# Kernel tuning notes

Hardware: AMD Instinct MI355X
Metric: run time of the kernel (lower is better)

## Reference

```python
import jax, jax.numpy as jnp
import numpy as np

B, C, T = 32, 64, 4096
K = 256  # truncated memory length (kwargs['k'])


def setup_inputs() -> dict:
    key = jax.random.key(0)
    k1, k2 = jax.random.split(key)
    x = jax.random.normal(k1, (B, C, T), dtype=jnp.float32)
    epsilon = jax.random.normal(k2, (), dtype=jnp.float32)
    loc = jnp.asarray(0.5, dtype=jnp.float32)    # alpha_loc parameter
    scale = jnp.asarray(0.1, dtype=jnp.float32)  # alpha_scale parameter (pre-softplus)
    return {"x": x, "loc": loc, "scale": scale, "epsilon": epsilon, "k": K}


def _gl_coeffs(alpha, k, dtype):
    # Grunwald-Letnikov weights: w_0 = 1, w_j = w_{j-1} * (j - 1 - alpha) / j
    j = jnp.arange(k, dtype=dtype)
    factors = jnp.where(j == 0, jnp.asarray(1.0, dtype),
                        (j - 1.0 - alpha) / jnp.maximum(j, 1.0))
    return jnp.cumprod(factors)  # [k]


def reference(x, loc, scale, epsilon, k):
    # reparameterized fractional order (Normal prior): alpha = loc + softplus(scale) * eps
    alpha = loc + jax.nn.softplus(scale) * epsilon
    w = _gl_coeffs(alpha, k, x.dtype)  # [k]
    b, c, t = x.shape
    # truncated GL fractional derivative = causal depthwise conv with k taps:
    # out[n] = sum_{j=0}^{k-1} w_j * x[n-j]
    lhs = x.reshape(b * c, 1, t)                 # [N, 1, T]
    rhs = w[::-1].reshape(1, 1, k)               # [O=1, I=1, K] (flip for correlation)
    out = jax.lax.conv_general_dilated(lhs, rhs, window_strides=(1,),
                                       padding=[(k - 1, 0)])
    return out.reshape(b, c, t)
```

## Files before the change

### kernel.cpp

```cpp
#include <hip/hip_runtime.h>
#include <hip/hip_bf16.h>
#include <hip/hip_fp16.h>

#define TLEN 4096
#define KTAPS 256
#define NT 18
#define WCH 24

typedef __attribute__((ext_vector_type(8))) _Float16 f16x8;
typedef __attribute__((ext_vector_type(4))) unsigned int uint4v;
typedef __attribute__((ext_vector_type(16))) float f32x16;

__global__ void __launch_bounds__(256, 5)
frac_conv_fused2(const float* __restrict__ x,
                 const float* __restrict__ loc,
                 const float* __restrict__ scale,
                 const float* __restrict__ eps,
                 float* __restrict__ out) {
    __shared__ __align__(16) float s[KTAPS];
    __shared__ unsigned int wrevp[320];
    __shared__ __align__(16) unsigned short Bf[WCH * 64 * 8];

    const int tid  = threadIdx.x;
    const int wave = tid >> 6;
    const int lane = tid & 63;
    const int l5   = lane >> 5;
    const int ln   = lane & 31;

    int wgid = blockIdx.x;
    if ((gridDim.x & 7) == 0) {
        const int cpx = gridDim.x >> 3;
        wgid = (blockIdx.x & 7) * cpx + (blockIdx.x >> 3);
    }
    const int rt  = wgid >> 5;
    const int sg  = wgid & 31;
    const int bn0 = sg * 128;

    const int r  = tid >> 3;
    const int cg = tid & 7;
    const float* __restrict__ xrow = x + (size_t)(rt * 32 + r) * TLEN;
    float4 v[12];
    #pragma unroll
    for (int jj = 0; jj < 12; ++jj) {
        const int w0 = cg * 4 + jj * 32;
        const int tg = bn0 - 256 + w0;
        v[jj] = (tg >= 0) ? *(const float4*)(xrow + tg) : make_float4(0.f, 0.f, 0.f, 0.f);
    }

    {
        const float alpha = loc[0] + log1pf(expf(scale[0])) * eps[0];
        const int j0 = 4 * lane;
        const float f0 = (j0 == 0) ? 1.0f : (((float)j0 - 1.0f - alpha) / (float)j0);
        const float f1 = (((float)j0 + 0.0f - alpha) / (float)(j0 + 1));
        const float f2 = (((float)j0 + 1.0f - alpha) / (float)(j0 + 2));
        const float f3 = (((float)j0 + 2.0f - alpha) / (float)(j0 + 3));
        const float p0 = f0, p1 = p0 * f1, p2 = p1 * f2, p3 = p2 * f3;
        float g = p3;
        #pragma unroll
        for (int dlt = 1; dlt < 64; dlt <<= 1) {
            const float t = __shfl_up(g, dlt, 64);
            if (lane >= dlt) g *= t;
        }
        float Sprev = __shfl_up(g, 1, 64);
        if (lane == 0) Sprev = 1.0f;
        if (wave == 0) {
            ((float4*)s)[lane] = make_float4(Sprev * p0, Sprev * p1, Sprev * p2, g);
        }
    }
    __syncthreads();

    {
        const int j = tid;
        const float a = (j >= 32) ? s[287 - j] : 0.0f;
        const float b = (j >= 31) ? s[286 - j] : 0.0f;
        wrevp[j] = __builtin_bit_cast(unsigned int, __builtin_amdgcn_cvt_pkrtz(a, b));
        if (tid < 64) {
            const int j2 = 256 + tid;
            const float a2 = (j2 <= 287) ? s[287 - j2] : 0.0f;
            const float b2 = (j2 <= 286) ? s[286 - j2] : 0.0f;
            wrevp[j2] = __builtin_bit_cast(unsigned int, __builtin_amdgcn_cvt_pkrtz(a2, b2));
        }
    }

    {
        uint2* Bf2 = (uint2*)Bf;
        #pragma unroll
        for (int jj = 0; jj < 12; ++jj) {
            const int w0 = cg * 4 + jj * 32;
            const auto a = __builtin_amdgcn_cvt_pkrtz(v[jj].x, v[jj].y);
            const auto b = __builtin_amdgcn_cvt_pkrtz(v[jj].z, v[jj].w);
            const int c  = w0 >> 4;
            const int h8 = (w0 >> 3) & 1;
            const int e0 = w0 & 7;
            const int uoff = (c * 64 + r + 32 * h8) * 8 + e0;
            Bf2[uoff >> 2] = make_uint2(__builtin_bit_cast(unsigned int, a),
                                        __builtin_bit_cast(unsigned int, b));
        }
    }
    __syncthreads();

    const int n0  = bn0 + wave * 32;
    const int lcb = wave * 2;
    const f16x8* Bv = (const f16x8*)Bf;
    const int o0 = 31 - ln + 8 * l5;

    auto LOADA = [&](int d) -> f16x8 {
        const int o = o0 + 16 * d;
        uint4v u;
        u[0] = wrevp[o];
        u[1] = wrevp[o + 2];
        u[2] = wrevp[o + 4];
        u[3] = wrevp[o + 6];
        return __builtin_bit_cast(f16x8, u);
    };

    f16x8 Afr[NT];
    f16x8 Bfr[NT];
    Bfr[0] = Bv[(lcb + 0) * 64 + lane];
    Bfr[1] = Bv[(lcb + 1) * 64 + lane];
    Bfr[2] = Bv[(lcb + 2) * 64 + lane];
    Bfr[3] = Bv[(lcb + 3) * 64 + lane];
    Afr[0] = LOADA(0);
    Afr[1] = LOADA(1);

    f32x16 acc = {0.f, 0.f, 0.f, 0.f, 0.f, 0.f, 0.f, 0.f,
                  0.f, 0.f, 0.f, 0.f, 0.f, 0.f, 0.f, 0.f};

    #pragma unroll
    for (int d = 0; d < NT; ++d) {
        if (d + 4 < NT) Bfr[d + 4] = Bv[(lcb + d + 4) * 64 + lane];
        if (d + 2 < NT) Afr[d + 2] = LOADA(d + 2);
        acc = __builtin_amdgcn_mfma_f32_32x32x16_f16(Afr[d], Bfr[d], acc, 0, 0, 0);
    }

    float* __restrict__ orow = out + (size_t)(rt * 32 + ln) * TLEN;
    #pragma unroll
    for (int g = 0; g < 4; ++g) {
        *(float4*)(orow + n0 + 8 * g + 4 * l5) =
            make_float4(acc[4 * g + 0], acc[4 * g + 1], acc[4 * g + 2], acc[4 * g + 3]);
    }
}

__global__ void gl_coeff_kernel(const float* __restrict__ loc,
                                const float* __restrict__ scale,
                                const float* __restrict__ eps,
                                float* __restrict__ w_out) {
    __shared__ float s[KTAPS];
    const int j = threadIdx.x;
    const float alpha = loc[0] + log1pf(expf(scale[0])) * eps[0];
    float f = (j == 0) ? 1.0f : (((float)j - 1.0f - alpha) / (float)j);
    s[j] = f;
    __syncthreads();
    #pragma unroll
    for (int st = 1; st < KTAPS; st <<= 1) {
        float v = s[j];
        float p = (j >= st) ? s[j - st] : 1.0f;
        __syncthreads();
        s[j] = v * p;
        __syncthreads();
    }
    w_out[j] = s[j];
}

__global__ void __launch_bounds__(256)
frac_conv_kernel(const float* __restrict__ x,
                 const float* __restrict__ w,
                 float* __restrict__ out) {
    __shared__ __align__(16) float xs[KTAPS + TLEN];
    __shared__ __align__(16) float wl[KTAPS];
    const int row = blockIdx.x;
    const int tid = threadIdx.x;
    const float* __restrict__ xr = x + (size_t)row * TLEN;
    float* __restrict__ orow = out + (size_t)row * TLEN;
    if (tid < 64) ((float4*)xs)[tid] = make_float4(0.f, 0.f, 0.f, 0.f);
    float4* xs4w = (float4*)(xs + KTAPS);
    const float4* xr4 = (const float4*)xr;
    #pragma unroll
    for (int k = 0; k < 4; ++k) xs4w[tid + k * 256] = xr4[tid + k * 256];
    if (tid < 64) ((float4*)wl)[tid] = ((const float4*)w)[tid];
    __syncthreads();
    const float4* __restrict__ xsv = (const float4*)xs;
    float4 acc[4]; float4 lo[4], hi[4]; int n0[4];
    #pragma unroll
    for (int g = 0; g < 4; ++g) {
        n0[g] = (tid << 2) + (g << 10);
        acc[g] = make_float4(0.f, 0.f, 0.f, 0.f);
        const int c = n0[g] >> 2;
        hi[g] = xsv[64 + c];
        lo[g] = xsv[63 + c];
    }
    #pragma unroll 4
    for (int j = 0; j < KTAPS - 4; j += 4) {
        const float4 w4 = *(const float4*)(wl + j);
        #pragma unroll
        for (int g = 0; g < 4; ++g) {
            acc[g].x += w4.x*hi[g].x + w4.y*lo[g].w + w4.z*lo[g].z + w4.w*lo[g].y;
            acc[g].y += w4.x*hi[g].y + w4.y*hi[g].x + w4.z*lo[g].w + w4.w*lo[g].z;
            acc[g].z += w4.x*hi[g].z + w4.y*hi[g].y + w4.z*hi[g].x + w4.w*lo[g].w;
            acc[g].w += w4.x*hi[g].w + w4.y*hi[g].z + w4.z*hi[g].y + w4.w*hi[g].x;
            hi[g] = lo[g];
            lo[g] = xsv[64 + ((n0[g] - j - 8) >> 2)];
        }
    }
    {
        const float4 w4 = *(const float4*)(wl + (KTAPS - 4));
        #pragma unroll
        for (int g = 0; g < 4; ++g) {
            acc[g].x += w4.x*hi[g].x + w4.y*lo[g].w + w4.z*lo[g].z + w4.w*lo[g].y;
            acc[g].y += w4.x*hi[g].y + w4.y*hi[g].x + w4.z*lo[g].w + w4.w*lo[g].z;
            acc[g].z += w4.x*hi[g].z + w4.y*hi[g].y + w4.z*hi[g].x + w4.w*lo[g].w;
            acc[g].w += w4.x*hi[g].w + w4.y*hi[g].z + w4.z*hi[g].y + w4.w*hi[g].x;
        }
    }
    #pragma unroll
    for (int g = 0; g < 4; ++g) *(float4*)(orow + n0[g]) = acc[g];
}

extern "C" void kernel_launch(void* const* d_in, const int* in_sizes, int n_in,
                              void* d_out, int out_size, void* d_ws, size_t ws_size,
                              hipStream_t stream) {
    const float* x     = (const float*)d_in[0];
    const float* loc   = (const float*)d_in[1];
    const float* scale = (const float*)d_in[2];
    const float* eps   = (const float*)d_in[3];
    float* out = (float*)d_out;
    const int rows = in_sizes[0] / TLEN;

    if ((rows % 32) == 0) {
        frac_conv_fused2<<<(rows / 32) * 32, 256, 0, stream>>>(x, loc, scale, eps, out);
    } else {
        float* w = (float*)d_ws;
        gl_coeff_kernel<<<1, 256, 0, stream>>>(loc, scale, eps, w);
        frac_conv_kernel<<<rows, 256, 0, stream>>>(x, w, out);
    }
}
```

Before: 19.77 us.

## Widen tiles to 512 columns with 8 waves and two MFMA accumulators per wave

Each block now covers 512 time steps per 32-row tile using 512 threads, and each wave computes two adjacent 32-column output tiles that share the same A (weight Toeplitz) fragments. This halves the halo overhead per output (256-sample halo over 512 instead of 128 columns) and reuses A loads across two MFMAs. Weight packing is done directly from wave 0 registers into the reversed fp16 buffer, removing the intermediate shared array and one barrier. The block remap to XCDs is also changed, and the larger block with more LDS may lower occupancy.

```diff
diff --git a/kernel.cpp b/kernel.cpp
--- a/kernel.cpp
+++ b/kernel.cpp
@@ -5,19 +5,22 @@
 #define TLEN 4096
 #define KTAPS 256
 #define NT 18
-#define WCH 24
+#define WCH 48
 
 typedef __attribute__((ext_vector_type(8))) _Float16 f16x8;
 typedef __attribute__((ext_vector_type(4))) unsigned int uint4v;
 typedef __attribute__((ext_vector_type(16))) float f32x16;
 
-__global__ void __launch_bounds__(256, 5)
-frac_conv_fused2(const float* __restrict__ x,
+static __device__ __forceinline__ unsigned int pkf16(float a, float b) {
+    return __builtin_bit_cast(unsigned int, __builtin_amdgcn_cvt_pkrtz(a, b));
+}
+
+__global__ void __launch_bounds__(512, 4)
+frac_conv_fused3(const float* __restrict__ x,
                  const float* __restrict__ loc,
                  const float* __restrict__ scale,
                  const float* __restrict__ eps,
                  float* __restrict__ out) {
-    __shared__ __align__(16) float s[KTAPS];
     __shared__ unsigned int wrevp[320];
     __shared__ __align__(16) unsigned short Bf[WCH * 64 * 8];
 
@@ -27,27 +30,33 @@
     const int l5   = lane >> 5;
     const int ln   = lane & 31;
 
-    int wgid = blockIdx.x;
-    if ((gridDim.x & 7) == 0) {
-        const int cpx = gridDim.x >> 3;
-        wgid = (blockIdx.x & 7) * cpx + (blockIdx.x >> 3);
-    }
-    const int rt  = wgid >> 5;
-    const int sg  = wgid & 31;
-    const int bn0 = sg * 128;
-
-    const int r  = tid >> 3;
-    const int cg = tid & 7;
+    int rt, sg;
+    {
+        const int bid = blockIdx.x;
+        if (gridDim.x == 512) {
+            const int xcd = bid & 7;
+            const int j   = bid >> 3;
+            rt = xcd * 8 + (j & 7);
+            sg = j >> 3;
+        } else {
+            rt = bid >> 3;
+            sg = bid & 7;
+        }
+    }
+    const int bn0 = sg * 512;
+
+    const int r  = tid >> 4;
+    const int cg = tid & 15;
     const float* __restrict__ xrow = x + (size_t)(rt * 32 + r) * TLEN;
     float4 v[12];
     #pragma unroll
     for (int jj = 0; jj < 12; ++jj) {
-        const int w0 = cg * 4 + jj * 32;
+        const int w0 = cg * 4 + jj * 64;
         const int tg = bn0 - 256 + w0;
         v[jj] = (tg >= 0) ? *(const float4*)(xrow + tg) : make_float4(0.f, 0.f, 0.f, 0.f);
     }
 
-    {
+    if (wave == 0) {
         const float alpha = loc[0] + log1pf(expf(scale[0])) * eps[0];
         const int j0 = 4 * lane;
         const float f0 = (j0 == 0) ? 1.0f : (((float)j0 - 1.0f - alpha) / (float)j0);
@@ -63,44 +72,36 @@
         }
         float Sprev = __shfl_up(g, 1, 64);
         if (lane == 0) Sprev = 1.0f;
-        if (wave == 0) {
-            ((float4*)s)[lane] = make_float4(Sprev * p0, Sprev * p1, Sprev * p2, g);
-        }
-    }
-    __syncthreads();
-
-    {
-        const int j = tid;
-        const float a = (j >= 32) ? s[287 - j] : 0.0f;
-        const float b = (j >= 31) ? s[286 - j] : 0.0f;
-        wrevp[j] = __builtin_bit_cast(unsigned int, __builtin_amdgcn_cvt_pkrtz(a, b));
-        if (tid < 64) {
-            const int j2 = 256 + tid;
-            const float a2 = (j2 <= 287) ? s[287 - j2] : 0.0f;
-            const float b2 = (j2 <= 286) ? s[286 - j2] : 0.0f;
-            wrevp[j2] = __builtin_bit_cast(unsigned int, __builtin_amdgcn_cvt_pkrtz(a2, b2));
-        }
+        const float q0 = Sprev * p0, q1 = Sprev * p1, q2 = Sprev * p2, q3 = g;
+        const float wm1 = (lane == 0) ? 0.0f : Sprev;
+        uint4v pk;
+        pk[0] = pkf16(q3, q2);
+        pk[1] = pkf16(q2, q1);
+        pk[2] = pkf16(q1, q0);
+        pk[3] = pkf16(q0, wm1);
+        *(uint4v*)(wrevp + 284 - 4 * lane) = pk;
+        if (lane == 63) wrevp[31] = pkf16(0.0f, q3);
+        if (lane < 31)  wrevp[lane] = 0u;
+        if (lane < 32)  wrevp[288 + lane] = 0u;
     }
 
     {
         uint2* Bf2 = (uint2*)Bf;
         #pragma unroll
         for (int jj = 0; jj < 12; ++jj) {
-            const int w0 = cg * 4 + jj * 32;
-            const auto a = __builtin_amdgcn_cvt_pkrtz(v[jj].x, v[jj].y);
-            const auto b = __builtin_amdgcn_cvt_pkrtz(v[jj].z, v[jj].w);
+            const int w0 = cg * 4 + jj * 64;
             const int c  = w0 >> 4;
             const int h8 = (w0 >> 3) & 1;
             const int e0 = w0 & 7;
             const int uoff = (c * 64 + r + 32 * h8) * 8 + e0;
-            Bf2[uoff >> 2] = make_uint2(__builtin_bit_cast(unsigned int, a),
-                                        __builtin_bit_cast(unsigned int, b));
+            Bf2[uoff >> 2] = make_uint2(pkf16(v[jj].x, v[jj].y),
+                                        pkf16(v[jj].z, v[jj].w));
         }
     }
     __syncthreads();
 
-    const int n0  = bn0 + wave * 32;
-    const int lcb = wave * 2;
+    const int n0  = bn0 + wave * 64;
+    const int lcb = wave * 4;
     const f16x8* Bv = (const f16x8*)Bf;
     const int o0 = 31 - ln + 8 * l5;
 
@@ -115,7 +116,7 @@
     };
 
     f16x8 Afr[NT];
-    f16x8 Bfr[NT];
+    f16x8 Bfr[NT + 2];
     Bfr[0] = Bv[(lcb + 0) * 64 + lane];
     Bfr[1] = Bv[(lcb + 1) * 64 + lane];
     Bfr[2] = Bv[(lcb + 2) * 64 + lane];
@@ -123,21 +124,25 @@
     Afr[0] = LOADA(0);
     Afr[1] = LOADA(1);
 
-    f32x16 acc = {0.f, 0.f, 0.f, 0.f, 0.f, 0.f, 0.f, 0.f,
-                  0.f, 0.f, 0.f, 0.f, 0.f, 0.f, 0.f, 0.f};
+    f32x16 acc0 = {0.f, 0.f, 0.f, 0.f, 0.f, 0.f, 0.f, 0.f,
+                   0.f, 0.f, 0.f, 0.f, 0.f, 0.f, 0.f, 0.f};
+    f32x16 acc1 = acc0;
 
     #pragma unroll
     for (int d = 0; d < NT; ++d) {
-        if (d + 4 < NT) Bfr[d + 4] = Bv[(lcb + d + 4) * 64 + lane];
-        if (d + 2 < NT) Afr[d + 2] = LOADA(d + 2);
-        acc = __builtin_amdgcn_mfma_f32_32x32x16_f16(Afr[d], Bfr[d], acc, 0, 0, 0);
+        if (d + 4 < NT + 2) Bfr[d + 4] = Bv[(lcb + d + 4) * 64 + lane];
+        if (d + 2 < NT)     Afr[d + 2] = LOADA(d + 2);
+        acc0 = __builtin_amdgcn_mfma_f32_32x32x16_f16(Afr[d], Bfr[d],     acc0, 0, 0, 0);
+        acc1 = __builtin_amdgcn_mfma_f32_32x32x16_f16(Afr[d], Bfr[d + 2], acc1, 0, 0, 0);
     }
 
     float* __restrict__ orow = out + (size_t)(rt * 32 + ln) * TLEN;
     #pragma unroll
     for (int g = 0; g < 4; ++g) {
         *(float4*)(orow + n0 + 8 * g + 4 * l5) =
-            make_float4(acc[4 * g + 0], acc[4 * g + 1], acc[4 * g + 2], acc[4 * g + 3]);
+            make_float4(acc0[4 * g + 0], acc0[4 * g + 1], acc0[4 * g + 2], acc0[4 * g + 3]);
+        *(float4*)(orow + n0 + 32 + 8 * g + 4 * l5) =
+            make_float4(acc1[4 * g + 0], acc1[4 * g + 1], acc1[4 * g + 2], acc1[4 * g + 3]);
     }
 }
 
@@ -227,7 +232,7 @@
     const int rows = in_sizes[0] / TLEN;
 
     if ((rows % 32) == 0) {
-        frac_conv_fused2<<<(rows / 32) * 32, 256, 0, stream>>>(x, loc, scale, eps, out);
+        frac_conv_fused3<<<(rows / 32) * 8, 512, 0, stream>>>(x, loc, scale, eps, out);
     } else {
         float* w = (float*)d_ws;
         gl_coeff_kernel<<<1, 256, 0, stream>>>(loc, scale, eps, w);
```

Result: faster. 18.90 us (-4.4%).
